# Performance work log

Hardware: AMD Instinct MI355X
Metric: run time of the kernel (lower is better)

The kernel has to match this reference:

```python
import jax, jax.numpy as jnp
import numpy as np

EPS = 1e-5
D = 32          # token embedding dim
HEADS = 8
DH = D // HEADS  # 4


def _layernorm(x, g, b):
    mu = jnp.mean(x, axis=-1, keepdims=True)
    var = jnp.mean(jnp.square(x - mu), axis=-1, keepdims=True)
    return (x - mu) / jnp.sqrt(var + EPS) * g + b


def _mhsa(x, Wqvk, W0):
    # x: [..., t, 32]; Wqvk: [96, 32]; W0: [32, 32]
    qkv = x @ Wqvk.T                                   # [..., t, 96]
    qkv = qkv.reshape(qkv.shape[:-1] + (DH, 3, HEADS))  # (d k h) layout of original rearrange
    q, k, v = qkv[..., 0, :], qkv[..., 1, :], qkv[..., 2, :]  # [..., t, d, h]
    scores = jnp.einsum('...tdh,...sdh->...hts', q, k) * (DH ** -0.5)
    attn = jax.nn.softmax(scores, axis=-1)
    out = jnp.einsum('...hts,...sdh->...thd', attn, v)  # [..., t, h, d]
    out = out.reshape(out.shape[:-2] + (D,))            # (h d) concat order
    return out @ W0.T


def setup_inputs() -> dict:
    key = jax.random.key(0)
    ks = jax.random.split(key, 8)
    B = 256
    s = D ** -0.5
    return {
        'x':       jax.random.normal(ks[0], (B, 3, 32, 32, 32), dtype=jnp.float32),
        'pos_y':   jax.random.normal(ks[1], (3, 32, 32), dtype=jnp.float32) * s,
        'Wqvk_y':  jax.random.normal(ks[2], (3, 3 * D, D), dtype=jnp.float32) * s,
        'W0_y':    jax.random.normal(ks[3], (3, D, D), dtype=jnp.float32) * s,
        'g_y':     jnp.ones((D,), dtype=jnp.float32),
        'b_y':     jnp.zeros((D,), dtype=jnp.float32),
        'Wqvk_x':  jax.random.normal(ks[4], (3, 3 * D, D), dtype=jnp.float32) * s,
        'W0_x':    jax.random.normal(ks[5], (3, D, D), dtype=jnp.float32) * s,
        'g_x':     jnp.ones((D,), dtype=jnp.float32),
        'b_x':     jnp.zeros((D,), dtype=jnp.float32),
    }


def reference(x, pos_y, Wqvk_y, W0_y, g_y, b_y, Wqvk_x, W0_x, g_x, b_x):
    # x: [b, 3, l, w, h] with l=w=h=32. Dropout layers are in eval mode (identity).
    tst = jnp.transpose(x, (0, 1, 4, 2, 3))               # [b, 3, i(=h), t(=l), d(=w)]
    # AbsPosEmb1D per RGB channel: in_ @ pos^T
    emb = jnp.einsum('bcitd,cjd->bcitj', tst, pos_y)      # [b, 3, 32, 32, 32]
    outs = []
    for c in range(3):  # distinct r/g/b weights
        o = _mhsa(emb[:, c], Wqvk_y[c], W0_y[c])
        outs.append(_layernorm(emb[:, c] + o, g_y, b_y))
    x_tmp = jnp.stack(outs, axis=1)                       # [b, 3, i, t, 32]
    x_tmp = jnp.transpose(x_tmp, (0, 1, 3, 4, 2))         # [b, 3, t, 32, i]
    x1 = jax.nn.sigmoid(x_tmp) * x                        # first gating

    # BUG in original second loop: it reuses the stale `emb_y` from the last
    # iteration of the first loop (channel b, i = width-1) for every (i, j).
    emb_last = emb[:, 2, -1]                              # [b, 32, 32]
    ys = []
    for c in range(3):
        o = _mhsa(emb_last, Wqvk_x[c], W0_x[c])
        ys.append(_layernorm(emb_last + o, g_x, b_x))
    tmp2 = jnp.stack(ys, axis=1)                          # [b, 3, t, 32]
    # y stacked over i (constant across i), then permuted to [b,3,32,i,32]
    y_perm = jnp.transpose(tmp2, (0, 1, 3, 2))[:, :, :, None, :]  # [b,3,32,1,32]
    return jax.nn.sigmoid(y_perm) * x1
```

## Files before the change

### kernel.cpp

```cpp
#include <hip/hip_runtime.h>
#include <hip/hip_bf16.h>


using bf16 = __hip_bfloat16;
typedef float v2f __attribute__((ext_vector_type(2)));
using short8 = __attribute__((ext_vector_type(8))) short;
using f32x4  = __attribute__((ext_vector_type(4))) float;

__device__ __forceinline__ v2f pk_fma(v2f acc, v2f a, v2f b) {
  asm("v_pk_fma_f32 %0, %1, %2, %0" : "+v"(acc) : "v"(a), "v"(b));
  return acc;
}

template <int CTRL>
__device__ __forceinline__ float dpp_add(float x) {
  return x + __int_as_float(
      __builtin_amdgcn_mov_dpp(__float_as_int(x), CTRL, 0xF, 0xF, true));
}

__device__ __forceinline__ ushort bf16_rne(float f) {
  uint u = __float_as_uint(f);
  return (ushort)((u + 0x7FFFu + ((u >> 16) & 1u)) >> 16);
}
__device__ __forceinline__ void split2(float x, ushort& h, ushort& l) {
  h = bf16_rne(x);
  l = bf16_rne(x - __uint_as_float((uint)h << 16));
}

__device__ __forceinline__ int frag_idx(int row, int k) {
  return ((row >> 4) << 9) + (((row & 15) + ((k >> 3) << 4)) << 3) + (k & 7);
}

struct __align__(16) SMem {
  ushort xsH[1024];
  ushort xsL[1024];
  union {
    ushort W[8192];
    struct {
      float esT[32][36];
      float aoF[32][36];
      float w0s[32][36];
    } s;
  } u;
  float qS[1024];
  float kT[1024];
  float vT[1024];
};

__device__ __forceinline__ float* swz_q(float* base, int t, int c) {
  return (float*)((char*)base + (((t << 7) + (c << 2)) ^ (((t >> 1) & 7) << 4)));
}
__device__ __forceinline__ const float* swz_qc(const float* base, int t, int c) {
  return (const float*)((const char*)base +
                        (((t << 7) + (c << 2)) ^ (((t >> 1) & 7) << 4)));
}
__device__ __forceinline__ float* swz_kv(float* base, int r, int s) {
  return (float*)((char*)base + (((r << 7) + (s << 2)) ^ ((r & 7) << 4)));
}
__device__ __forceinline__ const float* swz_kvc(const float* base, int r, int s) {
  return (const float*)((const char*)base +
                        (((r << 7) + (s << 2)) ^ ((r & 7) << 4)));
}

__global__ __launch_bounds__(256) void wc_kernel(
    const float* __restrict__ pos_y, const float* __restrict__ wqvk_y,
    const float* __restrict__ wqvk_x, ushort* __restrict__ wc2)
{
  const int n6 = blockIdx.x;
  const int c = n6 % 3, xset = n6 / 3;
  const float* W = (xset ? wqvk_x : wqvk_y) + c * 3072;
  const float* P = pos_y + (xset ? 2 : c) * 1024;
  __shared__ float Ws[96][33];
  __shared__ float Ps[32][33];
  const int tid = threadIdx.x;
#pragma unroll
  for (int k = 0; k < 12; ++k) {
    const int e = tid * 12 + k;
    Ws[e >> 5][e & 31] = W[e];
  }
#pragma unroll
  for (int k = 0; k < 4; ++k) {
    const int e = tid * 4 + k;
    Ps[e >> 5][e & 31] = P[e];
  }
  __syncthreads();
  const int n = tid & 127, half = tid >> 7;
  float src[16];
  if (n >= 96) {
    const int j = n - 96;
#pragma unroll
    for (int dd = 0; dd < 16; ++dd) src[dd] = Ps[j][16 * half + dd];
  } else {
    const int sidx = n >> 5;
    const int m = n & 31, dh = m & 3, h = m >> 2;
    const int f = dh * 24 + (sidx == 0 ? 8 : (sidx == 1 ? 16 : 0)) + h;
    const float sc = (sidx == 2) ? 0.72134752f : 1.0f;
#pragma unroll
    for (int dd = 0; dd < 16; ++dd) {
      float s = 0.f;
      for (int j = 0; j < 32; ++j) s += Ws[f][j] * Ps[j][16 * half + dd];
      src[dd] = s * sc;
    }
  }
  ushort* base = wc2 + (size_t)n6 * 8192;
  const int tile = n >> 4, rr = n & 15;
#pragma unroll
  for (int dd = 0; dd < 16; ++dd) {
    const int k = 16 * half + dd;
    const int off = tile * 512 + ((rr + ((k >> 3) << 4)) << 3) + (k & 7);
    ushort hh, ll;
    split2(src[dd], hh, ll);
    base[off]        = hh;
    base[4096 + off] = ll;
  }
}

__device__ __forceinline__ void load_tables(
    SMem& sm, int tid, const float* __restrict__ xbc, int i,
    const ushort* __restrict__ wc2)
{
  const int t = tid >> 3, dq = (tid & 7) * 4;
  float xv[4];
#pragma unroll
  for (int k = 0; k < 4; ++k) xv[k] = xbc[(t * 32 + dq + k) * 32 + i];
  ushort hs[4], ls[4];
#pragma unroll
  for (int k = 0; k < 4; ++k) split2(xv[k], hs[k], ls[k]);
  const int off = frag_idx(t, dq);
  *(short4*)&sm.xsH[off] = make_short4((short)hs[0], (short)hs[1],
                                       (short)hs[2], (short)hs[3]);
  *(short4*)&sm.xsL[off] = make_short4((short)ls[0], (short)ls[1],
                                       (short)ls[2], (short)ls[3]);
  {
    const float4* src = (const float4*)(wc2 + tid * 32);
    float4 r0 = src[0], r1 = src[1], r2 = src[2], r3 = src[3];
    float4* dst = (float4*)(sm.u.W + tid * 32);
    dst[0] = r0; dst[1] = r1; dst[2] = r2; dst[3] = r3;
  }
}

__device__ __forceinline__ void mhsa_core(SMem& sm, int tid,
                                          const float* __restrict__ w0g,
                                          float g0, float b0, float g1, float b1,
                                          float sig_out[2][2])
{
  const int wv = tid >> 6, lane = tid & 63;
  const int lr = lane & 15, lk = lane >> 4;
  const int mt = wv >> 1;
  const int qe = wv & 1;
  const int t0 = mt * 16 + lk * 4;
  f32x4 eC0 = {0.f,0.f,0.f,0.f}, eC1 = {0.f,0.f,0.f,0.f};

  {
    short8 aH = *(const short8*)&sm.xsH[mt * 512 + lane * 8];
    short8 aL = *(const short8*)&sm.xsL[mt * 512 + lane * 8];
    f32x4 acc[4];
#pragma unroll
    for (int q = 0; q < 4; ++q) {
      const int tile = qe * 4 + q;
      short8 bH = *(const short8*)&sm.u.W[tile * 512 + lane * 8];
      short8 bL = *(const short8*)&sm.u.W[4096 + tile * 512 + lane * 8];
      f32x4 c = {0.f, 0.f, 0.f, 0.f};
      c = __builtin_amdgcn_mfma_f32_16x16x32_bf16(aH, bH, c, 0, 0, 0);
      c = __builtin_amdgcn_mfma_f32_16x16x32_bf16(aH, bL, c, 0, 0, 0);
      c = __builtin_amdgcn_mfma_f32_16x16x32_bf16(aL, bH, c, 0, 0, 0);
      acc[q] = c;
    }
    if (qe == 0) {
      *(f32x4*)swz_kv(sm.kT, lr,      t0) = acc[0];
      *(f32x4*)swz_kv(sm.kT, lr + 16, t0) = acc[1];
      *(f32x4*)swz_kv(sm.vT, lr,      t0) = acc[2];
      *(f32x4*)swz_kv(sm.vT, lr + 16, t0) = acc[3];
    } else {
#pragma unroll
      for (int r = 0; r < 4; ++r) {
        *swz_q(sm.qS, t0 + r, lr)      = acc[0][r];
        *swz_q(sm.qS, t0 + r, lr + 16) = acc[1][r];
      }
      eC0 = acc[2]; eC1 = acc[3];
    }
  }
  float4 w0v = *(const float4*)&w0g[tid * 4];
  __syncthreads();
  if (qe == 1) {
    *(f32x4*)&sm.u.s.esT[lr][t0]      = eC0;
    *(f32x4*)&sm.u.s.esT[lr + 16][t0] = eC1;
  }
  { const int e = tid * 4; *(float4*)&sm.u.s.w0s[e >> 5][e & 31] = w0v; }

  {
    const int h = tid >> 5, tg2 = (tid >> 2) & 7, sg2 = tid & 3;
    const int ta = 4 * tg2, s0 = 8 * sg2;
    float4 qr0 = *(const float4*)swz_qc(sm.qS, ta + 0, 4 * h);
    float4 qr1 = *(const float4*)swz_qc(sm.qS, ta + 1, 4 * h);
    float4 qr2 = *(const float4*)swz_qc(sm.qS, ta + 2, 4 * h);
    float4 qr3 = *(const float4*)swz_qc(sm.qS, ta + 3, 4 * h);
    const float qa_[4][4] = {
        {qr0.x, qr0.y, qr0.z, qr0.w},
        {qr1.x, qr1.y, qr1.z, qr1.w},
        {qr2.x, qr2.y, qr2.z, qr2.w},
        {qr3.x, qr3.y, qr3.z, qr3.w}};
    v2f sc[4][4];
#pragma unroll
    for (int kk = 0; kk < 4; ++kk)
#pragma unroll
      for (int sp2 = 0; sp2 < 4; ++sp2) sc[kk][sp2] = v2f{0.f, 0.f};
#pragma unroll
    for (int dh = 0; dh < 4; ++dh) {
      float4 ka = *(const float4*)swz_kvc(sm.kT, 4 * h + dh, s0);
      float4 kb = *(const float4*)swz_kvc(sm.kT, 4 * h + dh, s0 + 4);
      v2f k0{ka.x, ka.y}, k1{ka.z, ka.w}, k2{kb.x, kb.y}, k3{kb.z, kb.w};
#pragma unroll
      for (int kk = 0; kk < 4; ++kk) {
        v2f qv{qa_[kk][dh], qa_[kk][dh]};
        sc[kk][0] = pk_fma(sc[kk][0], qv, k0);
        sc[kk][1] = pk_fma(sc[kk][1], qv, k1);
        sc[kk][2] = pk_fma(sc[kk][2], qv, k2);
        sc[kk][3] = pk_fma(sc[kk][3], qv, k3);
      }
    }
    float inv[4];
#pragma unroll
    for (int kk = 0; kk < 4; ++kk) {
#pragma unroll
      for (int sp2 = 0; sp2 < 4; ++sp2) {
        sc[kk][sp2][0] = exp2f(sc[kk][sp2][0]);
        sc[kk][sp2][1] = exp2f(sc[kk][sp2][1]);
      }
      v2f dv = sc[kk][0] + sc[kk][1];
      v2f dw = sc[kk][2] + sc[kk][3];
      dv += dw;
      float dn = dv[0] + dv[1];
      dn = dpp_add<0xB1>(dn);
      dn = dpp_add<0x4E>(dn);
      inv[kk] = __fdividef(1.0f, dn);
    }
    v2f pv[4][4];
#pragma unroll
    for (int kk = 0; kk < 4; ++kk)
#pragma unroll
      for (int dh = 0; dh < 4; ++dh) pv[kk][dh] = v2f{0.f, 0.f};
#pragma unroll
    for (int dh = 0; dh < 4; ++dh) {
      float4 va = *(const float4*)swz_kvc(sm.vT, 4 * h + dh, s0);
      float4 vb = *(const float4*)swz_kvc(sm.vT, 4 * h + dh, s0 + 4);
      v2f v0{va.x, va.y}, v1{va.z, va.w}, v2v{vb.x, vb.y}, v3{vb.z, vb.w};
#pragma unroll
      for (int kk = 0; kk < 4; ++kk) {
        pv[kk][dh] = pk_fma(pv[kk][dh], sc[kk][0], v0);
        pv[kk][dh] = pk_fma(pv[kk][dh], sc[kk][1], v1);
        pv[kk][dh] = pk_fma(pv[kk][dh], sc[kk][2], v2v);
        pv[kk][dh] = pk_fma(pv[kk][dh], sc[kk][3], v3);
      }
    }
    float ov[4][4];
#pragma unroll
    for (int kk = 0; kk < 4; ++kk)
#pragma unroll
      for (int dh = 0; dh < 4; ++dh) {
        float o = pv[kk][dh][0] + pv[kk][dh][1];
        o = dpp_add<0xB1>(o);
        o = dpp_add<0x4E>(o);
        ov[kk][dh] = o;
      }
    if (sg2 == 0) {
#pragma unroll
      for (int kk = 0; kk < 4; ++kk) {
        *(float4*)&sm.u.s.aoF[ta + kk][4 * h] = make_float4(
            ov[kk][0] * inv[kk], ov[kk][1] * inv[kk],
            ov[kk][2] * inv[kk], ov[kk][3] * inv[kk]);
      }
    }
  }
  __syncthreads();

  {
    const int g = tid >> 4, l = tid & 15;
    v2f a00{0.f,0.f}, a01{0.f,0.f}, a10{0.f,0.f}, a11{0.f,0.f};
#pragma unroll
    for (int f4 = 0; f4 < 8; ++f4) {
      float4 u0 = *(const float4*)&sm.u.s.aoF[g][4 * f4];
      float4 u1 = *(const float4*)&sm.u.s.aoF[g + 16][4 * f4];
      float4 w0 = *(const float4*)&sm.u.s.w0s[l][4 * f4];
      float4 w1 = *(const float4*)&sm.u.s.w0s[l + 16][4 * f4];
      a00 = pk_fma(a00, v2f{u0.x, u0.y}, v2f{w0.x, w0.y});
      a00 = pk_fma(a00, v2f{u0.z, u0.w}, v2f{w0.z, w0.w});
      a01 = pk_fma(a01, v2f{u0.x, u0.y}, v2f{w1.x, w1.y});
      a01 = pk_fma(a01, v2f{u0.z, u0.w}, v2f{w1.z, w1.w});
      a10 = pk_fma(a10, v2f{u1.x, u1.y}, v2f{w0.x, w0.y});
      a10 = pk_fma(a10, v2f{u1.z, u1.w}, v2f{w0.z, w0.w});
      a11 = pk_fma(a11, v2f{u1.x, u1.y}, v2f{w1.x, w1.y});
      a11 = pk_fma(a11, v2f{u1.z, u1.w}, v2f{w1.z, w1.w});
    }
    float rr[2][2];
    rr[0][0] = a00[0] + a00[1] + sm.u.s.esT[l][g];
    rr[0][1] = a01[0] + a01[1] + sm.u.s.esT[l + 16][g];
    rr[1][0] = a10[0] + a10[1] + sm.u.s.esT[l][g + 16];
    rr[1][1] = a11[0] + a11[1] + sm.u.s.esT[l + 16][g + 16];
    float s1a = rr[0][0] + rr[0][1], s1b = rr[1][0] + rr[1][1];
    float s2a = rr[0][0]*rr[0][0] + rr[0][1]*rr[0][1];
    float s2b = rr[1][0]*rr[1][0] + rr[1][1]*rr[1][1];
    s1a = dpp_add<0xB1>(s1a); s1a = dpp_add<0x4E>(s1a);
    s1a = dpp_add<0x124>(s1a); s1a = dpp_add<0x128>(s1a);
    s2a = dpp_add<0xB1>(s2a); s2a = dpp_add<0x4E>(s2a);
    s2a = dpp_add<0x124>(s2a); s2a = dpp_add<0x128>(s2a);
    s1b = dpp_add<0xB1>(s1b); s1b = dpp_add<0x4E>(s1b);
    s1b = dpp_add<0x124>(s1b); s1b = dpp_add<0x128>(s1b);
    s2b = dpp_add<0xB1>(s2b); s2b = dpp_add<0x4E>(s2b);
    s2b = dpp_add<0x124>(s2b); s2b = dpp_add<0x128>(s2b);
    const float mua = s1a * (1.0f / 32.0f), mub = s1b * (1.0f / 32.0f);
    const float ra = rsqrtf(s2a * (1.0f / 32.0f) - mua * mua + 1e-5f);
    const float rb = rsqrtf(s2b * (1.0f / 32.0f) - mub * mub + 1e-5f);
    sig_out[0][0] = __fdividef(1.0f, 1.0f + exp2f(-((rr[0][0] - mua) * ra * g0 + b0)));
    sig_out[0][1] = __fdividef(1.0f, 1.0f + exp2f(-((rr[0][1] - mua) * ra * g1 + b1)));
    sig_out[1][0] = __fdividef(1.0f, 1.0f + exp2f(-((rr[1][0] - mub) * rb * g0 + b0)));
    sig_out[1][1] = __fdividef(1.0f, 1.0f + exp2f(-((rr[1][1] - mub) * rb * g1 + b1)));
  }
}

__global__ __launch_bounds__(256, 5) void phase1_kernel(
    const float* __restrict__ x, const ushort* __restrict__ wc2,
    const float* __restrict__ w0_x,
    const float* __restrict__ g_x, const float* __restrict__ b_x,
    bf16* __restrict__ gates)
{
  __shared__ SMem sm;
  const int tid = threadIdx.x;
  const int n = blockIdx.x;
  const int c = n % 3, b = n / 3;
  const int l = tid & 15;
  const float L2E = 1.44269504f;
  const float g0 = g_x[l] * L2E,      b0 = b_x[l] * L2E;
  const float g1 = g_x[l + 16] * L2E, b1 = b_x[l + 16] * L2E;
  const float* xbc = x + (size_t)(b * 3 + 2) * 32768;
  load_tables(sm, tid, xbc, 31, wc2 + (size_t)(3 + c) * 8192);
  __syncthreads();
  float sig[2][2];
  mhsa_core(sm, tid, w0_x + c * 1024, g0, b0, g1, b1, sig);
  const int g = tid >> 4;
#pragma unroll
  for (int u = 0; u < 2; ++u)
#pragma unroll
    for (int v = 0; v < 2; ++v)
      gates[((c * 256 + b) * 32 + g + 16 * u) * 32 + l + 16 * v] =
          __float2bfloat16(sig[u][v]);
}

__global__ __launch_bounds__(256, 5) void phase2_kernel(
    const float* __restrict__ x, const ushort* __restrict__ wc2,
    const float* __restrict__ w0_y,
    const float* __restrict__ g_y, const float* __restrict__ b_y,
    const bf16* __restrict__ gates, float* __restrict__ out)
{
  __shared__ SMem sm;
  const int tid = threadIdx.x;
  const int n = blockIdx.x;
  const int p = (n & 7) * 3072 + (n >> 3);
  const int i = p & 31, bc = p >> 5;
  const int c = bc % 3, b = bc / 3;
  const int g = tid >> 4, l = tid & 15;
  const float L2E = 1.44269504f;
  const float g0 = g_y[l] * L2E,      b0 = b_y[l] * L2E;
  const float g1 = g_y[l + 16] * L2E, b1 = b_y[l + 16] * L2E;
  const int gbase = ((c * 256 + b) * 32 + i) * 32;
  const float sg0 = __bfloat162float(gates[gbase + g]);
  const float sg1 = __bfloat162float(gates[gbase + g + 16]);
  const float* xbc = x + (size_t)bc * 32768;
  load_tables(sm, tid, xbc, i, wc2 + (size_t)c * 8192);
  __syncthreads();
  float sig[2][2];
  mhsa_core(sm, tid, w0_y + c * 1024, g0, b0, g1, b1, sig);
  float* ob = out + (size_t)bc * 32768 + i;
#pragma unroll
  for (int u = 0; u < 2; ++u) {
    const int r = g + 16 * u;
    const float sgv = (u == 0) ? sg0 : sg1;
#pragma unroll
    for (int v = 0; v < 2; ++v) {
      const int cc = l + 16 * v;
      const int off = frag_idx(r, cc);
      const float xvv = __uint_as_float((uint)sm.xsH[off] << 16) +
                        __uint_as_float((uint)sm.xsL[off] << 16);
      ob[(r * 32 + cc) * 32] = sgv * sig[u][v] * xvv;
    }
  }
}

extern "C" void kernel_launch(void* const* d_in, const int* in_sizes, int n_in,
                              void* d_out, int out_size, void* d_ws, size_t ws_size,
                              hipStream_t stream) {
  const float* x      = (const float*)d_in[0];
  const float* pos_y  = (const float*)d_in[1];
  const float* wqvk_y = (const float*)d_in[2];
  const float* w0_y   = (const float*)d_in[3];
  const float* g_y    = (const float*)d_in[4];
  const float* b_y    = (const float*)d_in[5];
  const float* wqvk_x = (const float*)d_in[6];
  const float* w0_x   = (const float*)d_in[7];
  const float* g_x    = (const float*)d_in[8];
  const float* b_x    = (const float*)d_in[9];
  bf16*   gates = (bf16*)d_ws;
  ushort* wc2   = (ushort*)((char*)d_ws + 1572864);

  hipLaunchKernelGGL(wc_kernel, dim3(6), dim3(256), 0, stream,
                     pos_y, wqvk_y, wqvk_x, wc2);
  hipLaunchKernelGGL(phase1_kernel, dim3(768), dim3(256), 0, stream,
                     x, wc2, w0_x, g_x, b_x, gates);
  hipLaunchKernelGGL(phase2_kernel, dim3(24576), dim3(256), 0, stream,
                     x, wc2, w0_y, g_y, b_y, gates, (float*)d_out);
}
```

Before: 455.5 us.

## Process two i-slices per phase2 block sharing staged weights

Phase2 blocks now hold 512 threads and handle two adjacent i slices, each half owning its own x/q/k/v staging while both share one copy of the combined QKV weight table and W0 in LDS. The aim is to halve the weight staging and W0 loading done per slice. LayerNorm gamma/beta and gate values move from per-thread registers into padding columns of shared arrays. The XOR swizzles are replaced by padded rows, and an extra barrier is inserted after the q reads so the q buffer can be reused as the attention-output buffer. This raises LDS use per block and changes occupancy, and the padded layout may bring back bank conflicts.

```diff
diff --git a/kernel.cpp b/kernel.cpp
--- a/kernel.cpp
+++ b/kernel.cpp
@@ -31,36 +31,24 @@
   return ((row >> 4) << 9) + (((row & 15) + ((k >> 3) << 4)) << 3) + (k & 7);
 }
 
-struct __align__(16) SMem {
+struct __align__(16) Half {
   ushort xsH[1024];
   ushort xsL[1024];
   union {
+    float qS[32][36];
+    float aoF[32][36];
+  } qa;
+  float kT[32][36];
+  float vT[32][36];
+};
+
+struct __align__(16) SMem {
+  union {
     ushort W[8192];
-    struct {
-      float esT[32][36];
-      float aoF[32][36];
-      float w0s[32][36];
-    } s;
+    struct { float esT[2][32][36]; float w0s[32][36]; } o;
   } u;
-  float qS[1024];
-  float kT[1024];
-  float vT[1024];
+  Half h[2];
 };
-
-__device__ __forceinline__ float* swz_q(float* base, int t, int c) {
-  return (float*)((char*)base + (((t << 7) + (c << 2)) ^ (((t >> 1) & 7) << 4)));
-}
-__device__ __forceinline__ const float* swz_qc(const float* base, int t, int c) {
-  return (const float*)((const char*)base +
-                        (((t << 7) + (c << 2)) ^ (((t >> 1) & 7) << 4)));
-}
-__device__ __forceinline__ float* swz_kv(float* base, int r, int s) {
-  return (float*)((char*)base + (((r << 7) + (s << 2)) ^ ((r & 7) << 4)));
-}
-__device__ __forceinline__ const float* swz_kvc(const float* base, int r, int s) {
-  return (const float*)((const char*)base +
-                        (((r << 7) + (s << 2)) ^ ((r & 7) << 4)));
-}
 
 __global__ __launch_bounds__(256) void wc_kernel(
     const float* __restrict__ pos_y, const float* __restrict__ wqvk_y,
@@ -115,11 +103,10 @@
   }
 }
 
-__device__ __forceinline__ void load_tables(
-    SMem& sm, int tid, const float* __restrict__ xbc, int i,
-    const ushort* __restrict__ wc2)
+__device__ __forceinline__ void stage_x(Half& hh, int htid,
+                                        const float* __restrict__ xbc, int i)
 {
-  const int t = tid >> 3, dq = (tid & 7) * 4;
+  const int t = htid >> 3, dq = (htid & 7) * 4;
   float xv[4];
 #pragma unroll
   for (int k = 0; k < 4; ++k) xv[k] = xbc[(t * 32 + dq + k) * 32 + i];
@@ -127,24 +114,17 @@
 #pragma unroll
   for (int k = 0; k < 4; ++k) split2(xv[k], hs[k], ls[k]);
   const int off = frag_idx(t, dq);
-  *(short4*)&sm.xsH[off] = make_short4((short)hs[0], (short)hs[1],
+  *(short4*)&hh.xsH[off] = make_short4((short)hs[0], (short)hs[1],
                                        (short)hs[2], (short)hs[3]);
-  *(short4*)&sm.xsL[off] = make_short4((short)ls[0], (short)ls[1],
+  *(short4*)&hh.xsL[off] = make_short4((short)ls[0], (short)ls[1],
                                        (short)ls[2], (short)ls[3]);
-  {
-    const float4* src = (const float4*)(wc2 + tid * 32);
-    float4 r0 = src[0], r1 = src[1], r2 = src[2], r3 = src[3];
-    float4* dst = (float4*)(sm.u.W + tid * 32);
-    dst[0] = r0; dst[1] = r1; dst[2] = r2; dst[3] = r3;
-  }
-}
-
-__device__ __forceinline__ void mhsa_core(SMem& sm, int tid,
-                                          const float* __restrict__ w0g,
-                                          float g0, float b0, float g1, float b1,
+}
+
+__device__ __forceinline__ void mhsa_core(SMem& sm, Half& hh, int htid, int half,
+                                          const float* __restrict__ w0g, bool lead,
                                           float sig_out[2][2])
 {
-  const int wv = tid >> 6, lane = tid & 63;
+  const int wv = htid >> 6, lane = htid & 63;
   const int lr = lane & 15, lk = lane >> 4;
   const int mt = wv >> 1;
   const int qe = wv & 1;
@@ -152,8 +132,8 @@
   f32x4 eC0 = {0.f,0.f,0.f,0.f}, eC1 = {0.f,0.f,0.f,0.f};
 
   {
-    short8 aH = *(const short8*)&sm.xsH[mt * 512 + lane * 8];
-    short8 aL = *(const short8*)&sm.xsL[mt * 512 + lane * 8];
+    short8 aH = *(const short8*)&hh.xsH[mt * 512 + lane * 8];
+    short8 aL = *(const short8*)&hh.xsL[mt * 512 + lane * 8];
     f32x4 acc[4];
 #pragma unroll
     for (int q = 0; q < 4; ++q) {
@@ -167,34 +147,36 @@
       acc[q] = c;
     }
     if (qe == 0) {
-      *(f32x4*)swz_kv(sm.kT, lr,      t0) = acc[0];
-      *(f32x4*)swz_kv(sm.kT, lr + 16, t0) = acc[1];
-      *(f32x4*)swz_kv(sm.vT, lr,      t0) = acc[2];
-      *(f32x4*)swz_kv(sm.vT, lr + 16, t0) = acc[3];
+      *(f32x4*)&hh.kT[lr][t0]      = acc[0];
+      *(f32x4*)&hh.kT[lr + 16][t0] = acc[1];
+      *(f32x4*)&hh.vT[lr][t0]      = acc[2];
+      *(f32x4*)&hh.vT[lr + 16][t0] = acc[3];
     } else {
 #pragma unroll
       for (int r = 0; r < 4; ++r) {
-        *swz_q(sm.qS, t0 + r, lr)      = acc[0][r];
-        *swz_q(sm.qS, t0 + r, lr + 16) = acc[1][r];
+        hh.qa.qS[t0 + r][lr]      = acc[0][r];
+        hh.qa.qS[t0 + r][lr + 16] = acc[1][r];
       }
       eC0 = acc[2]; eC1 = acc[3];
     }
   }
-  float4 w0v = *(const float4*)&w0g[tid * 4];
+  float4 w0v = make_float4(0.f, 0.f, 0.f, 0.f);
+  if (lead) w0v = *(const float4*)&w0g[htid * 4];
   __syncthreads();
   if (qe == 1) {
-    *(f32x4*)&sm.u.s.esT[lr][t0]      = eC0;
-    *(f32x4*)&sm.u.s.esT[lr + 16][t0] = eC1;
-  }
-  { const int e = tid * 4; *(float4*)&sm.u.s.w0s[e >> 5][e & 31] = w0v; }
+    *(f32x4*)&sm.u.o.esT[half][lr][t0]      = eC0;
+    *(f32x4*)&sm.u.o.esT[half][lr + 16][t0] = eC1;
+  }
+  if (lead) { const int e = htid * 4; *(float4*)&sm.u.o.w0s[e >> 5][e & 31] = w0v; }
 
   {
-    const int h = tid >> 5, tg2 = (tid >> 2) & 7, sg2 = tid & 3;
+    const int h2 = htid >> 5, tg2 = (htid >> 2) & 7, sg2 = htid & 3;
     const int ta = 4 * tg2, s0 = 8 * sg2;
-    float4 qr0 = *(const float4*)swz_qc(sm.qS, ta + 0, 4 * h);
-    float4 qr1 = *(const float4*)swz_qc(sm.qS, ta + 1, 4 * h);
-    float4 qr2 = *(const float4*)swz_qc(sm.qS, ta + 2, 4 * h);
-    float4 qr3 = *(const float4*)swz_qc(sm.qS, ta + 3, 4 * h);
+    float4 qr0 = *(const float4*)&hh.qa.qS[ta + 0][4 * h2];
+    float4 qr1 = *(const float4*)&hh.qa.qS[ta + 1][4 * h2];
+    float4 qr2 = *(const float4*)&hh.qa.qS[ta + 2][4 * h2];
+    float4 qr3 = *(const float4*)&hh.qa.qS[ta + 3][4 * h2];
+    __syncthreads();
     const float qa_[4][4] = {
         {qr0.x, qr0.y, qr0.z, qr0.w},
         {qr1.x, qr1.y, qr1.z, qr1.w},
@@ -207,8 +189,9 @@
       for (int sp2 = 0; sp2 < 4; ++sp2) sc[kk][sp2] = v2f{0.f, 0.f};
 #pragma unroll
     for (int dh = 0; dh < 4; ++dh) {
-      float4 ka = *(const float4*)swz_kvc(sm.kT, 4 * h + dh, s0);
-      float4 kb = *(const float4*)swz_kvc(sm.kT, 4 * h + dh, s0 + 4);
+      const float* kr = &hh.kT[4 * h2 + dh][s0];
+      float4 ka = *(const float4*)&kr[0];
+      float4 kb = *(const float4*)&kr[4];
       v2f k0{ka.x, ka.y}, k1{ka.z, ka.w}, k2{kb.x, kb.y}, k3{kb.z, kb.w};
 #pragma unroll
       for (int kk = 0; kk < 4; ++kk) {
@@ -242,8 +225,9 @@
       for (int dh = 0; dh < 4; ++dh) pv[kk][dh] = v2f{0.f, 0.f};
 #pragma unroll
     for (int dh = 0; dh < 4; ++dh) {
-      float4 va = *(const float4*)swz_kvc(sm.vT, 4 * h + dh, s0);
-      float4 vb = *(const float4*)swz_kvc(sm.vT, 4 * h + dh, s0 + 4);
+      const float* vr = &hh.vT[4 * h2 + dh][s0];
+      float4 va = *(const float4*)&vr[0];
+      float4 vb = *(const float4*)&vr[4];
       v2f v0{va.x, va.y}, v1{va.z, va.w}, v2v{vb.x, vb.y}, v3{vb.z, vb.w};
 #pragma unroll
       for (int kk = 0; kk < 4; ++kk) {
@@ -266,7 +250,7 @@
     if (sg2 == 0) {
 #pragma unroll
       for (int kk = 0; kk < 4; ++kk) {
-        *(float4*)&sm.u.s.aoF[ta + kk][4 * h] = make_float4(
+        *(float4*)&hh.qa.aoF[ta + kk][4 * h2] = make_float4(
             ov[kk][0] * inv[kk], ov[kk][1] * inv[kk],
             ov[kk][2] * inv[kk], ov[kk][3] * inv[kk]);
       }
@@ -275,14 +259,14 @@
   __syncthreads();
 
   {
-    const int g = tid >> 4, l = tid & 15;
+    const int g = htid >> 4, l = htid & 15;
     v2f a00{0.f,0.f}, a01{0.f,0.f}, a10{0.f,0.f}, a11{0.f,0.f};
 #pragma unroll
     for (int f4 = 0; f4 < 8; ++f4) {
-      float4 u0 = *(const float4*)&sm.u.s.aoF[g][4 * f4];
-      float4 u1 = *(const float4*)&sm.u.s.aoF[g + 16][4 * f4];
-      float4 w0 = *(const float4*)&sm.u.s.w0s[l][4 * f4];
-      float4 w1 = *(const float4*)&sm.u.s.w0s[l + 16][4 * f4];
+      float4 u0 = *(const float4*)&hh.qa.aoF[g][4 * f4];
+      float4 u1 = *(const float4*)&hh.qa.aoF[g + 16][4 * f4];
+      float4 w0 = *(const float4*)&sm.u.o.w0s[l][4 * f4];
+      float4 w1 = *(const float4*)&sm.u.o.w0s[l + 16][4 * f4];
       a00 = pk_fma(a00, v2f{u0.x, u0.y}, v2f{w0.x, w0.y});
       a00 = pk_fma(a00, v2f{u0.z, u0.w}, v2f{w0.z, w0.w});
       a01 = pk_fma(a01, v2f{u0.x, u0.y}, v2f{w1.x, w1.y});
@@ -293,10 +277,10 @@
       a11 = pk_fma(a11, v2f{u1.z, u1.w}, v2f{w1.z, w1.w});
     }
     float rr[2][2];
-    rr[0][0] = a00[0] + a00[1] + sm.u.s.esT[l][g];
-    rr[0][1] = a01[0] + a01[1] + sm.u.s.esT[l + 16][g];
-    rr[1][0] = a10[0] + a10[1] + sm.u.s.esT[l][g + 16];
-    rr[1][1] = a11[0] + a11[1] + sm.u.s.esT[l + 16][g + 16];
+    rr[0][0] = a00[0] + a00[1] + sm.u.o.esT[half][l][g];
+    rr[0][1] = a01[0] + a01[1] + sm.u.o.esT[half][l + 16][g];
+    rr[1][0] = a10[0] + a10[1] + sm.u.o.esT[half][l][g + 16];
+    rr[1][1] = a11[0] + a11[1] + sm.u.o.esT[half][l + 16][g + 16];
     float s1a = rr[0][0] + rr[0][1], s1b = rr[1][0] + rr[1][1];
     float s2a = rr[0][0]*rr[0][0] + rr[0][1]*rr[0][1];
     float s2b = rr[1][0]*rr[1][0] + rr[1][1]*rr[1][1];
@@ -311,6 +295,8 @@
     const float mua = s1a * (1.0f / 32.0f), mub = s1b * (1.0f / 32.0f);
     const float ra = rsqrtf(s2a * (1.0f / 32.0f) - mua * mua + 1e-5f);
     const float rb = rsqrtf(s2b * (1.0f / 32.0f) - mub * mub + 1e-5f);
+    const float g0 = hh.qa.qS[l][32],      b0 = hh.qa.qS[l][33];
+    const float g1 = hh.qa.qS[l + 16][32], b1 = hh.qa.qS[l + 16][33];
     sig_out[0][0] = __fdividef(1.0f, 1.0f + exp2f(-((rr[0][0] - mua) * ra * g0 + b0)));
     sig_out[0][1] = __fdividef(1.0f, 1.0f + exp2f(-((rr[0][1] - mua) * ra * g1 + b1)));
     sig_out[1][0] = __fdividef(1.0f, 1.0f + exp2f(-((rr[1][0] - mub) * rb * g0 + b0)));
@@ -318,7 +304,7 @@
   }
 }
 
-__global__ __launch_bounds__(256, 5) void phase1_kernel(
+__global__ __launch_bounds__(256, 4) void phase1_kernel(
     const float* __restrict__ x, const ushort* __restrict__ wc2,
     const float* __restrict__ w0_x,
     const float* __restrict__ g_x, const float* __restrict__ b_x,
@@ -326,18 +312,26 @@
 {
   __shared__ SMem sm;
   const int tid = threadIdx.x;
+  Half& hh = sm.h[0];
   const int n = blockIdx.x;
   const int c = n % 3, b = n / 3;
-  const int l = tid & 15;
-  const float L2E = 1.44269504f;
-  const float g0 = g_x[l] * L2E,      b0 = b_x[l] * L2E;
-  const float g1 = g_x[l + 16] * L2E, b1 = b_x[l + 16] * L2E;
   const float* xbc = x + (size_t)(b * 3 + 2) * 32768;
-  load_tables(sm, tid, xbc, 31, wc2 + (size_t)(3 + c) * 8192);
+  {
+    const float4* src = (const float4*)(wc2 + (size_t)(3 + c) * 8192 + tid * 32);
+    float4 r0 = src[0], r1 = src[1], r2 = src[2], r3 = src[3];
+    float4* dst = (float4*)(sm.u.W + tid * 32);
+    dst[0] = r0; dst[1] = r1; dst[2] = r2; dst[3] = r3;
+  }
+  stage_x(hh, tid, xbc, 31);
+  if (tid < 32) {
+    const float L2E = 1.44269504f;
+    hh.qa.qS[tid][32] = g_x[tid] * L2E;
+    hh.qa.qS[tid][33] = b_x[tid] * L2E;
+  }
   __syncthreads();
   float sig[2][2];
-  mhsa_core(sm, tid, w0_x + c * 1024, g0, b0, g1, b1, sig);
-  const int g = tid >> 4;
+  mhsa_core(sm, hh, tid, 0, w0_x + c * 1024, true, sig);
+  const int g = tid >> 4, l = tid & 15;
 #pragma unroll
   for (int u = 0; u < 2; ++u)
 #pragma unroll
@@ -346,7 +340,7 @@
           __float2bfloat16(sig[u][v]);
 }
 
-__global__ __launch_bounds__(256, 5) void phase2_kernel(
+__global__ __launch_bounds__(512, 6) void phase2_kernel(
     const float* __restrict__ x, const ushort* __restrict__ wc2,
     const float* __restrict__ w0_y,
     const float* __restrict__ g_y, const float* __restrict__ b_y,
@@ -354,33 +348,43 @@
 {
   __shared__ SMem sm;
   const int tid = threadIdx.x;
+  const int half = tid >> 8, htid = tid & 255;
+  Half& hh = sm.h[half];
   const int n = blockIdx.x;
-  const int p = (n & 7) * 3072 + (n >> 3);
-  const int i = p & 31, bc = p >> 5;
+  const int p = (n & 7) * 1536 + (n >> 3);
+  const int ii = p & 15, bc = p >> 4;
   const int c = bc % 3, b = bc / 3;
-  const int g = tid >> 4, l = tid & 15;
-  const float L2E = 1.44269504f;
-  const float g0 = g_y[l] * L2E,      b0 = b_y[l] * L2E;
-  const float g1 = g_y[l + 16] * L2E, b1 = b_y[l + 16] * L2E;
-  const int gbase = ((c * 256 + b) * 32 + i) * 32;
-  const float sg0 = __bfloat162float(gates[gbase + g]);
-  const float sg1 = __bfloat162float(gates[gbase + g + 16]);
+  const int i = ii * 2 + half;
   const float* xbc = x + (size_t)bc * 32768;
-  load_tables(sm, tid, xbc, i, wc2 + (size_t)c * 8192);
+  {
+    const float4* src = (const float4*)(wc2 + (size_t)c * 8192 + tid * 16);
+    float4 r0 = src[0], r1 = src[1];
+    float4* dst = (float4*)(sm.u.W + tid * 16);
+    dst[0] = r0; dst[1] = r1;
+  }
+  stage_x(hh, htid, xbc, i);
+  if (htid < 32) {
+    const float L2E = 1.44269504f;
+    hh.qa.qS[htid][32] = g_y[htid] * L2E;
+    hh.qa.qS[htid][33] = b_y[htid] * L2E;
+    hh.kT[htid][32] =
+        __bfloat162float(gates[((c * 256 + b) * 32 + i) * 32 + htid]);
+  }
   __syncthreads();
   float sig[2][2];
-  mhsa_core(sm, tid, w0_y + c * 1024, g0, b0, g1, b1, sig);
+  mhsa_core(sm, hh, htid, half, w0_y + c * 1024, half == 0, sig);
+  const int g = htid >> 4, l = htid & 15;
   float* ob = out + (size_t)bc * 32768 + i;
 #pragma unroll
   for (int u = 0; u < 2; ++u) {
     const int r = g + 16 * u;
-    const float sgv = (u == 0) ? sg0 : sg1;
+    const float sgv = hh.kT[r][32];
 #pragma unroll
     for (int v = 0; v < 2; ++v) {
       const int cc = l + 16 * v;
       const int off = frag_idx(r, cc);
-      const float xvv = __uint_as_float((uint)sm.xsH[off] << 16) +
-                        __uint_as_float((uint)sm.xsL[off] << 16);
+      const float xvv = __uint_as_float((uint)hh.xsH[off] << 16) +
+                        __uint_as_float((uint)hh.xsL[off] << 16);
       ob[(r * 32 + cc) * 32] = sgv * sig[u][v] * xvv;
     }
   }
@@ -406,6 +410,6 @@
                      pos_y, wqvk_y, wqvk_x, wc2);
   hipLaunchKernelGGL(phase1_kernel, dim3(768), dim3(256), 0, stream,
                      x, wc2, w0_x, g_x, b_x, gates);
-  hipLaunchKernelGGL(phase2_kernel, dim3(24576), dim3(256), 0, stream,
+  hipLaunchKernelGGL(phase2_kernel, dim3(12288), dim3(512), 0, stream,
                      x, wc2, w0_y, g_y, b_y, gates, (float*)d_out);
 }
```

Result: faster. 406.6 us (-10.7%).
